# Kernel tuning notes

Hardware: AMD Instinct MI355X
Metric: run time of the kernel (lower is better)

## Reference

```python
import jax, jax.numpy as jnp
from jax import lax
import numpy as np
from functools import partial

B, C, H, W = 4, 3, 256, 256
HW = H * W
KCAP = 32          # max tracked components per (batch, class) slot
MAX_ITER = 5
KSIZE = 5


def _depthwise_sum(x, k):
    c = x.shape[1]
    w = jnp.ones((c, 1, k, k), x.dtype)
    return lax.conv_general_dilated(x, w, (1, 1), [(k // 2, k // 2)] * 2,
                                    feature_group_count=c,
                                    dimension_numbers=('NCHW', 'OIHW', 'NCHW'))


def erode(x):
    return (_depthwise_sum(x, KSIZE) >= KSIZE * KSIZE - 0.5).astype(x.dtype)


def dilate(x):
    return (_depthwise_sum(x, KSIZE) > 0.5).astype(x.dtype)


def _maxpool3_int(L):
    return lax.reduce_window(L, jnp.int32(0), lax.max, (1, 1, 3, 3), (1, 1, 1, 1),
                             [(0, 0), (0, 0), (1, 1), (1, 1)])


def label_cc(binary):
    # connected-component labeling by iterated 3x3 max-pool of pixel indices,
    # exactly as find_components_max_pool (labels = max flat pixel index in comp)
    b = lax.stop_gradient(binary) > 0.5
    idx = jnp.arange(HW, dtype=jnp.int32).reshape(1, 1, H, W)
    L0 = jnp.where(b, idx, 0)

    def cond(st):
        return st[1]

    def body(st):
        L, _ = st
        Ln = jnp.where(b, _maxpool3_int(L), 0)
        return Ln, jnp.any(Ln != L)

    L, _ = lax.while_loop(cond, body, (L0, jnp.array(True)))
    return L


def extract_components(Lf, binf):
    # per (b,c): top-KCAP components sorted by comp.sum() = size*label/maxL (desc)
    flat = Lf.reshape(-1)
    sizes = jnp.zeros((HW,), jnp.float32).at[flat].add(binf.reshape(-1))
    idx = jnp.arange(HW, dtype=jnp.int32)
    is_root = (flat == idx) & (flat > 0)  # label 0 excluded, as in torch code
    key = jnp.where(is_root, lax.stop_gradient(sizes) * idx.astype(jnp.float32), -1.0)
    _, top_lab = lax.top_k(key, KCAP)
    valid = key[top_lab] > 0.0
    maxL = jnp.maximum(flat.max(), 1).astype(jnp.float32)
    v = top_lab.astype(jnp.float32)
    s = jnp.where(valid, sizes[top_lab] * v / maxL, 0.0)  # comp.sum()
    lab = jnp.where(valid, top_lab, -1)
    # component tensor = mask * label/maxL, exactly mask*L/max(L) of the original
    comps = (Lf[None] == lab[:, None, None]).astype(jnp.float32) * (v / maxL)[:, None, None]
    return s, comps, valid


def process_step(P, n, bar, s, comps, valid, t):
    # overlaps vs components stored BEFORE this step; new comps within a step
    # are pixel-disjoint so they can never match each other (overlap == 0).
    OV = jnp.einsum('jhw,khw->jk', comps, P)

    def body(carry, inp):
        P, n, bar = carry
        s_j, comp_j, valid_j, ov_j = inp
        best = jnp.argmax(ov_j)
        matched = ov_j[best] > 0.0
        widx = jnp.clip(jnp.where(matched, best, n), 0, KCAP - 1)
        can = valid_j & (matched | (n < KCAP))
        bar = bar.at[widx, t].set(jnp.where(can, s_j, bar[widx, t]))
        add = valid_j & (~matched) & (n < KCAP)
        nw = jnp.minimum(n, KCAP - 1)
        P = P.at[nw].set(jnp.where(add, comp_j, P[nw]))
        return (P, n + add.astype(n.dtype), bar), None

    (P, n, bar), _ = lax.scan(body, (P, n, bar), (s, comps, valid, OV))
    return P, n, bar


def compute_barcodes(binary):
    half = MAX_ITER // 2
    seq = [(binary, half)]
    m = binary
    for t in range(half):
        m = erode(m)
        seq.append((m, half + t + 1))
    m = binary
    for t in range(half):
        m = dilate(m)
        seq.append((m, half - t - 1))
    BC = B * C
    P = jnp.zeros((BC, KCAP, H, W), jnp.float32)
    n = jnp.zeros((BC,), jnp.int32)
    bar = jnp.zeros((BC, KCAP, MAX_ITER), jnp.float32)
    for mp, t in seq:  # fixed 5-step schedule (structural loop)
        L = label_cc(mp).reshape(BC, H, W)
        s, comps, valid = jax.vmap(extract_components)(L, mp.reshape(BC, H, W))
        P, n, bar = jax.vmap(partial(process_step, t=t))(P, n, bar, s, comps, valid)
    return bar.reshape(B, C, KCAP, MAX_ITER), n.reshape(B, C)


def topo_forward(predictions, gumbel, targets):
    y_soft = jax.nn.softmax(predictions + gumbel, axis=1)
    hard = jax.nn.one_hot(jnp.argmax(y_soft, axis=1), C, axis=1, dtype=jnp.float32)
    binary_pred = hard + y_soft - lax.stop_gradient(y_soft)  # straight-through
    binary_tgt = jnp.moveaxis(jax.nn.one_hot(targets, C, dtype=jnp.float32), -1, 1)
    bp, n_p = compute_barcodes(binary_pred)
    bt, n_t = compute_barcodes(binary_tgt)
    k = jnp.arange(KCAP)
    valid_p = k[None, None] < n_p[:, :, None]
    has_t = k[None, None] < n_t[:, :, None]
    pmax = bp.max(-1)
    pmax = jnp.where(pmax > 0, pmax, 1.0)
    tgt = jnp.where(has_t[..., None], bt, 0.0)
    term = jnp.sum((tgt - bp) ** 2, -1) / pmax ** 2
    losses = jnp.sum(jnp.where(valid_p, term, 0.0), axis=(1, 2))
    return losses.mean()  # reduction='mean'


def setup_inputs() -> dict:
    key = jax.random.key(0)
    k1, k2, k3 = jax.random.split(key, 3)
    # blob-like logits: low-res noise upsampled so component counts stay < KCAP
    lo = jax.random.normal(k1, (B, C, 16, 16), jnp.float32)
    predictions = 8.0 * jax.image.resize(lo, (B, C, H, W), 'linear')
    lo_t = jax.random.normal(k2, (B, C, 16, 16), jnp.float32)
    targets = jnp.argmax(jax.image.resize(lo_t, (B, C, H, W), 'linear'), axis=1).astype(jnp.int32)
    u = jax.random.uniform(k3, (B, C, H, W), jnp.float32, minval=1e-6, maxval=1.0 - 1e-6)
    gumbel = -jnp.log(-jnp.log(u))  # standard Gumbel noise (F.gumbel_softmax)
    return {"predictions": predictions, "gumbel": gumbel, "targets": targets}


def reference(predictions, gumbel, targets):
    return topo_forward(predictions, gumbel, targets)
```

## Files before the change

### kernel.cpp

```cpp
#include <hip/hip_runtime.h>

#define NB 4
#define NC 3
#define BC 12
#define HW 65536
#define KCAP 32
#define MAXI 5
#define RUNCAP 16384
#define NSLOT 120
#define NCH 24

typedef unsigned long long u64;
typedef unsigned int u32;

__device__ __forceinline__ int uf_find(int* P, int x){
  while (true){
    int p = P[x];
    if (p == x) return x;
    int gp = P[p];
    if (gp == p) return p;
    P[x] = gp;
    x = gp;
  }
}
__device__ __forceinline__ void uf_union_max(int* P, int a, int b){
  while (true){
    a = uf_find(P, a); b = uf_find(P, b);
    if (a == b) return;
    if (a > b){ int t = a; a = b; b = t; }
    int old = atomicCAS(&P[a], a, b);
    if (old == a) return;
    a = old;
  }
}

template<typename F>
__device__ __forceinline__ void walk_runs(const u64* wv, F&& emit){
  int open_s = -1;
  #pragma unroll
  for (int wi = 0; wi < 4; wi++){
    u64 v = wv[wi];
    int base = wi << 6;
    int pos = 0;
    while (pos < 64){
      u64 rem = v >> pos;
      if (open_s >= 0){
        u64 nz = ~rem;
        int z = nz ? __builtin_ctzll(nz) : 64;
        if (z >= 64 - pos){ pos = 64; }
        else { emit(open_s, base + pos + z); open_s = -1; pos += z; }
      } else {
        if (rem == 0ull){ pos = 64; }
        else {
          int o = __builtin_ctzll(rem);
          open_s = base + pos + o;
          pos += o;
        }
      }
    }
  }
  if (open_s >= 0) emit(open_s, 256);
}

__global__ void k_bin(const float* __restrict__ pred, const float* __restrict__ gum,
                      const int* __restrict__ tgt, u64* __restrict__ bmAll){
  int g = blockIdx.x * 256 + threadIdx.x;
  int b = g >> 16, p = g & (HW - 1);
  size_t base = (size_t)b * NC * HW + p;
  float v0 = pred[base]        + gum[base];
  float v1 = pred[base + HW]   + gum[base + HW];
  float v2 = pred[base + 2*HW] + gum[base + 2*HW];
  int a = 0; float m = v0;
  if (v1 > m){ m = v1; a = 1; }
  if (v2 > m){ m = v2; a = 2; }
  int tg = tgt[(size_t)b * HW + p];
  u64 p0 = __ballot(a == 0), p1 = __ballot(a == 1), p2 = __ballot(a == 2);
  u64 t0 = __ballot(tg == 0), t1 = __ballot(tg == 1), t2 = __ballot(tg == 2);
  if ((threadIdx.x & 63) == 0){
    int w = p >> 6;
    int sp = b * NC;
    bmAll[(size_t)(sp + 0) * 1024 + w] = p0;
    bmAll[(size_t)(sp + 1) * 1024 + w] = p1;
    bmAll[(size_t)(sp + 2) * 1024 + w] = p2;
    int st = 60 + b * NC;
    bmAll[(size_t)(st + 0) * 1024 + w] = t0;
    bmAll[(size_t)(st + 1) * 1024 + w] = t1;
    bmAll[(size_t)(st + 2) * 1024 + w] = t2;
  }
}

__global__ void k_morph4(const u64* __restrict__ bmAll, u64* __restrict__ bmAllW,
                         int4 srcs, int4 dsts, int4 flgs){
  int t = blockIdx.x * 256 + threadIdx.x;
  int job = t / 12288, rest = t % 12288;
  int s = rest >> 10, word = rest & 1023;
  int row = word >> 2, w = word & 3;
  int srcG = job == 0 ? srcs.x : job == 1 ? srcs.y : job == 2 ? srcs.z : srcs.w;
  int dstG = job == 0 ? dsts.x : job == 1 ? dsts.y : job == 2 ? dsts.z : dsts.w;
  int er   = job == 0 ? flgs.x : job == 1 ? flgs.y : job == 2 ? flgs.z : flgs.w;
  const u64* bs = bmAll + (size_t)(srcG * BC + s) * 1024;
  u64 res = er ? ~0ull : 0ull;
  for (int dy = -2; dy <= 2; dy++){
    int y = row + dy;
    if (y < 0 || y > 255){ if (er) res = 0; continue; }
    const u64* rw = bs + y * 4;
    u64 m = rw[w];
    u64 l = (w > 0) ? rw[w-1] : 0ull;
    u64 r = (w < 3) ? rw[w+1] : 0ull;
    u64 x1l = (m << 1) | (l >> 63);
    u64 x2l = (m << 2) | (l >> 62);
    u64 x1r = (m >> 1) | (r << 63);
    u64 x2r = (m >> 2) | (r << 62);
    u64 h = er ? (m & x1l & x2l & x1r & x2r) : (m | x1l | x2l | x1r | x2r);
    res = er ? (res & h) : (res | h);
  }
  bmAllW[(size_t)(dstG * BC + s) * 1024 + word] = res;
}

__global__ __launch_bounds__(1024) void k_cc_runs(
    const u64* __restrict__ bmAll, u32* __restrict__ selRuns,
    int* __restrict__ selCnt, float* __restrict__ sSel, float* __restrict__ scaleSel){
  __shared__ int par[RUNCAP];
  __shared__ u32 pkz[RUNCAP];
  __shared__ int rs[257];
  __shared__ u64 wcand[16*KCAP];
  __shared__ u64 selKeys[KCAP];
  __shared__ int selRoot[KCAP];
  __shared__ int wsum[4], wsum2[4];
  __shared__ int lmS;
  int u = blockIdx.x, t = threadIdx.x;
  int lane = t & 63, wid = t >> 6;
  bool rowT = t < 256;
  u64 wv[4] = {0,0,0,0};
  int nr = 0;
  if (rowT){
    const u64* bp = bmAll + (size_t)u * 1024 + t * 4;
    #pragma unroll
    for (int i = 0; i < 4; i++) wv[i] = bp[i];
    walk_runs(wv, [&](int a, int b){ (void)a; (void)b; nr++; });
  }
  if (t == 0) lmS = 0;
  {
    int v = nr;
    #pragma unroll
    for (int d = 1; d < 64; d <<= 1){
      int o = __shfl_up(v, d);
      if (lane >= d) v += o;
    }
    if (rowT && lane == 63) wsum[wid] = v;
    __syncthreads();
    if (rowT){
      int pre = 0;
      for (int q = 0; q < wid; q++) pre += wsum[q];
      rs[t] = pre + v - nr;
      if (t == 255) rs[256] = pre + v;
    }
    __syncthreads();
  }
  int NR = rs[256];
  int NRc = NR < RUNCAP ? NR : RUNCAP;
  int myBase = rowT ? rs[t] : 0;
  for (int i = t; i < NRc; i += 1024) par[i] = i;
  if (rowT){
    int o = myBase;
    walk_runs(wv, [&](int a, int b){
      if (o < RUNCAP) pkz[o] = ((u32)t << 16) | ((u32)a << 8) | (u32)(b - 1);
      o++;
    });
  }
  __syncthreads();
  for (int i = t; i < NRc; i += 1024){
    u32 v = pkz[i];
    int r = v >> 16;
    if (r == 0) continue;
    int s2 = (int)((v >> 8) & 255), E2 = (int)(v & 255);
    int a0 = rs[r-1], a1 = rs[r];
    if (a1 > NRc) a1 = NRc;
    if (a0 >= a1) continue;
    int lo = a0, hi = a1;
    while (lo < hi){
      int mid = (lo + hi) >> 1;
      if ((int)(pkz[mid] & 255) >= s2 - 1) hi = mid; else lo = mid + 1;
    }
    for (int j = lo; j < a1; j++){
      int s1 = (int)((pkz[j] >> 8) & 255);
      if (s1 > E2 + 1) break;
      uf_union_max(par, i, j);
    }
  }
  __syncthreads();
  for (int i = t; i < NRc; i += 1024){
    int r = i, p = par[r];
    while (p != r){ r = p; p = par[r]; }
    par[i] = r;
  }
  __syncthreads();
  {
    int lm = 0;
    for (int i0 = 0; i0 < NRc; i0 += 1024){
      int i = i0 + t;
      int root = -1, len = 0;
      if (i < NRc){
        u32 v = pkz[i];
        int s0 = (int)((v >> 8) & 255), E = (int)(v & 255);
        len = E - s0 + 1;
        root = par[i] & 16383;
        lm = max(lm, (int)(v >> 16) * 256 + E);
      }
      int val = len;
      int prev = __shfl_up(root, 1);
      unsigned flg = (lane == 0 || prev != root) ? 1u : 0u;
      #pragma unroll
      for (int d = 1; d < 64; d <<= 1){
        int ov = __shfl_up(val, d);
        unsigned of = __shfl_up(flg, d);
        if (lane >= d){
          if (!flg) val += ov;
          flg |= of;
        }
      }
      int nroot = __shfl_down(root, 1);
      bool last = (lane == 63) || (nroot != root);
      if (i < NRc && last) atomicAdd(&par[root], val << 14);
    }
    #pragma unroll
    for (int off = 32; off > 0; off >>= 1) lm = max(lm, __shfl_xor(lm, off));
    if (lane == 0) atomicMax(&lmS, lm);
  }
  __syncthreads();
  float maxLf = (float)(lmS >= 1 ? lmS : 1);
  for (int i = t; i < NRc; i += 1024){
    int pv = par[i];
    if ((pv & 16383) == i){
      u32 v = pkz[i];
      int lab = (int)(v >> 16) * 256 + (int)(v & 255);
      if (lab > 0){
        float key = (float)((u32)pv >> 14) * (float)lab;
        pkz[i] = __float_as_uint(key);
        par[i] = (lab << 14) | i;
      } else {
        pkz[i] = 0;
      }
    }
  }
  __syncthreads();
  {
    u64 myBest = 0;
    for (int i = t; i < NRc; i += 1024){
      int pv = par[i];
      if ((pv & 16383) != i) continue;
      u32 kh = pkz[i];
      if (!kh) continue;
      u64 cand = ((u64)kh << 32) | ((u64)(0xFFFFu - ((u32)pv >> 14)) << 16) | (u64)i;
      if (cand > myBest) myBest = cand;
    }
    if (lane < KCAP) wcand[wid*KCAP + lane] = 0;
    for (int r = 0; r < KCAP; r++){
      u64 b = myBest;
      #pragma unroll
      for (int off = 32; off > 0; off >>= 1){
        u64 o = __shfl_xor(b, off);
        b = (o > b) ? o : b;
      }
      if (b == 0) break;
      if (lane == 0) wcand[wid*KCAP + r] = b;
      if (myBest == b){
        pkz[(int)(b & 16383)] = 0;
        myBest = 0;
        for (int i = t; i < NRc; i += 1024){
          int pv = par[i];
          if ((pv & 16383) != i) continue;
          u32 kh = pkz[i];
          if (!kh) continue;
          u64 cand = ((u64)kh << 32) | ((u64)(0xFFFFu - ((u32)pv >> 14)) << 16) | (u64)i;
          if (cand > myBest) myBest = cand;
        }
      }
    }
  }
  __syncthreads();
  if (wid == 0){
    u64 c[8];
    #pragma unroll
    for (int q = 0; q < 8; q++) c[q] = wcand[q*64 + lane];
    if (lane < KCAP) selKeys[lane] = 0;
    for (int r = 0; r < KCAP; r++){
      u64 b = 0;
      #pragma unroll
      for (int q = 0; q < 8; q++) b = (c[q] > b) ? c[q] : b;
      #pragma unroll
      for (int off = 32; off > 0; off >>= 1){
        u64 o = __shfl_xor(b, off);
        b = (o > b) ? o : b;
      }
      if (b == 0) break;
      #pragma unroll
      for (int q = 0; q < 8; q++) if (c[q] == b) c[q] = 0;
      if (lane == 0) selKeys[r] = b;
    }
  }
  __syncthreads();
  if (t < KCAP){
    u64 k = selKeys[t];
    if (k){
      int lab = 0xFFFF - (int)((k >> 16) & 0xFFFF);
      selRoot[t] = (int)(k & 0x3FFF);
      sSel[u*KCAP + t]     = __uint_as_float((u32)(k >> 32)) / maxLf;
      scaleSel[u*KCAP + t] = (float)lab / maxLf;
    } else {
      selRoot[t] = -1;
      sSel[u*KCAP + t] = 0.0f;
      scaleSel[u*KCAP + t] = 0.0f;
    }
  }
  __syncthreads();
  for (int i = t; i < NRc; i += 1024) pkz[i] = 255u;
  __syncthreads();
  if (t < KCAP && selRoot[t] >= 0) pkz[selRoot[t]] = (u32)t;
  __syncthreads();
  int c = 0;
  if (rowT){
    int o = myBase;
    walk_runs(wv, [&](int a, int b){
      if (o < RUNCAP && pkz[par[o] & 16383] < KCAP) c++;
      o++;
    });
  }
  {
    int v = c;
    #pragma unroll
    for (int d = 1; d < 64; d <<= 1){
      int o = __shfl_up(v, d);
      if (lane >= d) v += o;
    }
    if (rowT && lane == 63) wsum2[wid] = v;
    __syncthreads();
    if (rowT){
      int pre = 0;
      for (int q = 0; q < wid; q++) pre += wsum2[q];
      int w = pre + v - c;
      size_t base = (size_t)u * RUNCAP;
      int o = myBase;
      walk_runs(wv, [&](int a, int b){
        if (o < RUNCAP){
          u32 j = pkz[par[o] & 16383];
          if (j < KCAP){
            selRuns[base + w] = (j << 24) | ((u32)t << 16) | ((u32)a << 8) | (u32)(b - 1);
            w++;
          }
        }
        o++;
      });
    }
    if (t == 0) selCnt[u] = wsum2[0] + wsum2[1] + wsum2[2] + wsum2[3];
  }
}

__global__ __launch_bounds__(1024) void k_chainall(
    const u32* __restrict__ selRuns, const int* __restrict__ selCnt,
    const float* __restrict__ sSel, const float* __restrict__ scaleSel,
    float* __restrict__ barP, float* __restrict__ barT,
    int* __restrict__ n24, u64* __restrict__ PbT){
  int w = blockIdx.x, t = threadIdx.x;
  int pass = w / 12, s = w % 12;
  __shared__ int cnt[16*KCAP*KCAP];
  __shared__ float spL[KCAP];
  __shared__ int add_dst[KCAP];
  __shared__ int bestA[KCAP];
  __shared__ float bvA[KCAP];
  __shared__ int nS;
  if (t < KCAP) spL[t] = 0.0f;
  if (t == 0) nS = 0;
  float* bar = (pass ? barT : barP) + (size_t)s * KCAP * MAXI;
  u64* Pb = PbT + (size_t)w * KCAP * 1024;
  int g = t >> 5, k = t & 31;
  int wid = t >> 6;
  #pragma unroll 1
  for (int st = 0; st < 5; st++){
    int u = (pass * 5 + st) * BC + s;
    int tval = (st < 3) ? st + 2 : (st == 3 ? 1 : 0);
    for (int i = t; i < 16*KCAP*KCAP; i += 1024) cnt[i] = 0;
    __syncthreads();
    int n0 = nS;
    int NS = selCnt[u];
    const u32* rp = selRuns + (size_t)u * RUNCAP;
    if (n0 > 0){
      for (int i = g; i < NS; i += 32){
        u32 v = rp[i];
        int j = v >> 24;
        int row = (v >> 16) & 255, s0 = (v >> 8) & 255, E = (int)(v & 255);
        int w0 = s0 >> 6, w1 = E >> 6;
        int acc = 0;
        if (k < n0){
          for (int wi = w0; wi <= w1; wi++){
            int lo = max(s0, wi << 6), hi = min(E + 1, (wi << 6) + 64);
            u64 mask = (hi - lo == 64) ? ~0ull : ((((u64)1 << (hi - lo)) - 1) << (lo - (wi << 6)));
            acc += __popcll(Pb[(size_t)(row * 4 + wi) * KCAP + k] & mask);
          }
          if (acc) atomicAdd(&cnt[wid*KCAP*KCAP + j*KCAP + k], acc);
        }
      }
    }
    __syncthreads();
    {
      int tot = 0;
      #pragma unroll
      for (int wq = 0; wq < 16; wq++) tot += cnt[wq*KCAP*KCAP + t];
      cnt[t] = tot;
    }
    __syncthreads();
    if (t < KCAP){
      float sn = scaleSel[(size_t)u*KCAP + t];
      int best = 0; float bv = 0.0f;
      if (sn > 0.0f && n0 > 0){
        bv = sn * spL[0] * (float)cnt[t*KCAP + 0];
        for (int k2 = 1; k2 < n0; k2++){
          float ov = sn * spL[k2] * (float)cnt[t*KCAP + k2];
          if (ov > bv){ bv = ov; best = k2; }
        }
      }
      bestA[t] = best; bvA[t] = bv;
    }
    __syncthreads();
    if (t == 0){
      int n = n0;
      for (int j = 0; j < KCAP; j++){
        add_dst[j] = -1;
        float sv = scaleSel[(size_t)u*KCAP + j];
        if (sv <= 0.0f) continue;
        if (bvA[j] > 0.0f){
          bar[bestA[j]*MAXI + tval] = sSel[(size_t)u*KCAP + j];
        } else if (n < KCAP){
          bar[n*MAXI + tval] = sSel[(size_t)u*KCAP + j];
          spL[n] = sv;
          add_dst[j] = n;
          n++;
        }
      }
      nS = n;
    }
    __syncthreads();
    for (int j = 0; j < KCAP; j++){
      int d = add_dst[j];
      if (d < 0) continue;
      for (int x = t; x < 1024; x += 1024) Pb[(size_t)x * KCAP + d] = 0ull;
    }
    __syncthreads();
    for (int i = t; i < NS; i += 1024){
      u32 v = rp[i];
      int j = v >> 24;
      int d = add_dst[j];
      if (d < 0) continue;
      int row = (v >> 16) & 255, s0 = (v >> 8) & 255, E = (int)(v & 255);
      int w0 = s0 >> 6, w1 = E >> 6;
      for (int wi = w0; wi <= w1; wi++){
        int lo = max(s0, wi << 6), hi = min(E + 1, (wi << 6) + 64);
        u64 mask = (hi - lo == 64) ? ~0ull : ((((u64)1 << (hi - lo)) - 1) << (lo - (wi << 6)));
        atomicOr(&Pb[(size_t)(row * 4 + wi) * KCAP + d], mask);
      }
    }
    __syncthreads();
  }
  if (t == 0) n24[w] = nS;
}

__global__ void k_loss(const float* __restrict__ barP, const float* __restrict__ barT,
                       const int* __restrict__ n24, float* __restrict__ out){
  __shared__ float red[512];
  int t = threadIdx.x;
  float val = 0.0f;
  if (t < BC * KCAP){
    int s = t >> 5, k = t & 31;
    int np = n24[s], nt = n24[12 + s];
    if (k < np){
      const float* bp = barP + (size_t)(s*KCAP + k)*MAXI;
      float pmax = bp[0];
      #pragma unroll
      for (int q = 1; q < MAXI; q++) pmax = fmaxf(pmax, bp[q]);
      if (!(pmax > 0.0f)) pmax = 1.0f;
      float acc = 0.0f;
      #pragma unroll
      for (int q = 0; q < MAXI; q++){
        float tv = (k < nt) ? barT[(size_t)(s*KCAP + k)*MAXI + q] : 0.0f;
        float d = tv - bp[q];
        acc += d * d;
      }
      val = acc / (pmax * pmax);
    }
  }
  red[t] = val;
  __syncthreads();
  for (int off = 256; off > 0; off >>= 1){
    if (t < off) red[t] += red[t + off];
    __syncthreads();
  }
  if (t == 0) out[0] = red[0] * 0.25f;
}

extern "C" void kernel_launch(void* const* d_in, const int* in_sizes, int n_in,
                              void* d_out, int out_size, void* d_ws, size_t ws_size,
                              hipStream_t stream){
  const float* pred = (const float*)d_in[0];
  const float* gum  = (const float*)d_in[1];
  const int*   tgt  = (const int*)d_in[2];
  float* out = (float*)d_out;
  char* ws = (char*)d_ws;
  size_t off = 0;
  auto alloc = [&](size_t bytes)->char*{
    char* p = ws + off;
    off += (bytes + 255) & ~(size_t)255;
    return p;
  };
  u64* bmAll   = (u64*)alloc((size_t)NSLOT*1024*8);
  u32* selRuns = (u32*)alloc((size_t)NSLOT*RUNCAP*4);
  int* selCnt  = (int*)alloc(NSLOT*4);
  float* sSel     = (float*)alloc((size_t)NSLOT*KCAP*4);
  float* scaleSel = (float*)alloc((size_t)NSLOT*KCAP*4);
  u64* PbT     = (u64*)alloc((size_t)NCH*KCAP*1024*8);
  int* n24     = (int*)alloc(NCH*4);
  size_t zbytes = (size_t)(BC*KCAP*MAXI*2)*4;
  char* zreg = alloc(zbytes);
  float* barP = (float*)zreg;
  float* barT = barP + BC*KCAP*MAXI;
  if (off > ws_size) return;

  hipMemsetAsync(zreg, 0, zbytes, stream);
  k_bin<<<(NB*HW)/256,256,0,stream>>>(pred, gum, tgt, bmAll);
  k_morph4<<<192,256,0,stream>>>(bmAll, bmAll, make_int4(0,0,5,5), make_int4(1,3,6,8), make_int4(1,0,1,0));
  k_morph4<<<192,256,0,stream>>>(bmAll, bmAll, make_int4(1,3,6,8), make_int4(2,4,7,9), make_int4(1,0,1,0));
  k_cc_runs<<<NSLOT,1024,0,stream>>>(bmAll, selRuns, selCnt, sSel, scaleSel);
  k_chainall<<<NCH,1024,0,stream>>>(selRuns, selCnt, sSel, scaleSel, barP, barT, n24, PbT);
  k_loss<<<1,512,0,stream>>>(barP, barT, n24, out);
}
```

Measured before the change: 308.6 us.

## Build new component bitmasks in LDS and unroll overlap run loop by four

```diff
diff --git a/kernel.cpp b/kernel.cpp
--- a/kernel.cpp
+++ b/kernel.cpp
@@ -356,25 +356,27 @@
   }
 }
 
-__global__ __launch_bounds__(1024) void k_chainall(
+__global__ __launch_bounds__(1024, 4) void k_chainall(
     const u32* __restrict__ selRuns, const int* __restrict__ selCnt,
     const float* __restrict__ sSel, const float* __restrict__ scaleSel,
     float* __restrict__ barP, float* __restrict__ barT,
     int* __restrict__ n24, u64* __restrict__ PbT){
   int w = blockIdx.x, t = threadIdx.x;
   int pass = w / 12, s = w % 12;
-  __shared__ int cnt[16*KCAP*KCAP];
+  __shared__ u64 shbuf[8192];
   __shared__ float spL[KCAP];
   __shared__ int add_dst[KCAP];
   __shared__ int bestA[KCAP];
   __shared__ float bvA[KCAP];
   __shared__ int nS;
+  int* cnt = (int*)shbuf;
   if (t < KCAP) spL[t] = 0.0f;
   if (t == 0) nS = 0;
   float* bar = (pass ? barT : barP) + (size_t)s * KCAP * MAXI;
   u64* Pb = PbT + (size_t)w * KCAP * 1024;
   int g = t >> 5, k = t & 31;
   int wid = t >> 6;
+  int cw = wid * KCAP * KCAP;
   #pragma unroll 1
   for (int st = 0; st < 5; st++){
     int u = (pass * 5 + st) * BC + s;
@@ -384,28 +386,41 @@
     int n0 = nS;
     int NS = selCnt[u];
     const u32* rp = selRuns + (size_t)u * RUNCAP;
+    #define OVRUN(vv, jj, aacc) { \
+      jj = (int)((vv) >> 24); aacc = 0; \
+      if (jj < KCAP && k < n0){ \
+        int row_ = ((vv) >> 16) & 255, s0_ = ((vv) >> 8) & 255, E_ = (int)((vv) & 255); \
+        int w0_ = s0_ >> 6, w1_ = E_ >> 6; \
+        for (int wi_ = w0_; wi_ <= w1_; wi_++){ \
+          int lo_ = max(s0_, wi_ << 6), hi_ = min(E_ + 1, (wi_ << 6) + 64); \
+          u64 m_ = (hi_ - lo_ == 64) ? ~0ull : ((((u64)1 << (hi_ - lo_)) - 1) << (lo_ - (wi_ << 6))); \
+          aacc += __popcll(Pb[(size_t)(row_ * 4 + wi_) * KCAP + k] & m_); \
+        } \
+      } }
     if (n0 > 0){
-      for (int i = g; i < NS; i += 32){
-        u32 v = rp[i];
-        int j = v >> 24;
-        int row = (v >> 16) & 255, s0 = (v >> 8) & 255, E = (int)(v & 255);
-        int w0 = s0 >> 6, w1 = E >> 6;
-        int acc = 0;
-        if (k < n0){
-          for (int wi = w0; wi <= w1; wi++){
-            int lo = max(s0, wi << 6), hi = min(E + 1, (wi << 6) + 64);
-            u64 mask = (hi - lo == 64) ? ~0ull : ((((u64)1 << (hi - lo)) - 1) << (lo - (wi << 6)));
-            acc += __popcll(Pb[(size_t)(row * 4 + wi) * KCAP + k] & mask);
-          }
-          if (acc) atomicAdd(&cnt[wid*KCAP*KCAP + j*KCAP + k], acc);
-        }
-      }
-    }
+      for (int i = g; i < NS; i += 128){
+        u32 va = rp[i];
+        u32 vb = (i + 32 < NS) ? rp[i + 32] : 0xFFFFFFFFu;
+        u32 vc = (i + 64 < NS) ? rp[i + 64] : 0xFFFFFFFFu;
+        u32 vd = (i + 96 < NS) ? rp[i + 96] : 0xFFFFFFFFu;
+        int j0, j1, j2, j3, a0, a1, a2, a3;
+        OVRUN(va, j0, a0);
+        OVRUN(vb, j1, a1);
+        OVRUN(vc, j2, a2);
+        OVRUN(vd, j3, a3);
+        if (a0) atomicAdd(&cnt[cw + j0*KCAP + k], a0);
+        if (a1) atomicAdd(&cnt[cw + j1*KCAP + k], a1);
+        if (a2) atomicAdd(&cnt[cw + j2*KCAP + k], a2);
+        if (a3) atomicAdd(&cnt[cw + j3*KCAP + k], a3);
+      }
+    }
+    #undef OVRUN
     __syncthreads();
     {
       int tot = 0;
       #pragma unroll
       for (int wq = 0; wq < 16; wq++) tot += cnt[wq*KCAP*KCAP + t];
+      __syncthreads();
       cnt[t] = tot;
     }
     __syncthreads();
@@ -440,24 +455,29 @@
       nS = n;
     }
     __syncthreads();
-    for (int j = 0; j < KCAP; j++){
-      int d = add_dst[j];
-      if (d < 0) continue;
-      for (int x = t; x < 1024; x += 1024) Pb[(size_t)x * KCAP + d] = 0ull;
-    }
-    __syncthreads();
-    for (int i = t; i < NS; i += 1024){
-      u32 v = rp[i];
-      int j = v >> 24;
-      int d = add_dst[j];
-      if (d < 0) continue;
-      int row = (v >> 16) & 255, s0 = (v >> 8) & 255, E = (int)(v & 255);
-      int w0 = s0 >> 6, w1 = E >> 6;
-      for (int wi = w0; wi <= w1; wi++){
-        int lo = max(s0, wi << 6), hi = min(E + 1, (wi << 6) + 64);
-        u64 mask = (hi - lo == 64) ? ~0ull : ((((u64)1 << (hi - lo)) - 1) << (lo - (wi << 6)));
-        atomicOr(&Pb[(size_t)(row * 4 + wi) * KCAP + d], mask);
-      }
+    int nTot = nS;
+    for (int b0 = n0; b0 < nTot; b0 += 8){
+      int bcnt = min(8, nTot - b0);
+      for (int x = t; x < 8192; x += 1024) shbuf[x] = 0ull;
+      __syncthreads();
+      for (int i = t; i < NS; i += 1024){
+        u32 v = rp[i];
+        int j = v >> 24;
+        if (j >= KCAP) continue;
+        int d = add_dst[j];
+        if (d < b0 || d >= b0 + bcnt) continue;
+        int row = (v >> 16) & 255, s0 = (v >> 8) & 255, E = (int)(v & 255);
+        int w0 = s0 >> 6, w1 = E >> 6;
+        for (int wi = w0; wi <= w1; wi++){
+          int lo = max(s0, wi << 6), hi = min(E + 1, (wi << 6) + 64);
+          u64 mask = (hi - lo == 64) ? ~0ull : ((((u64)1 << (hi - lo)) - 1) << (lo - (wi << 6)));
+          atomicOr(&shbuf[(size_t)(row * 4 + wi) * 8 + (d - b0)], mask);
+        }
+      }
+      __syncthreads();
+      for (int dd = 0; dd < bcnt; dd++)
+        Pb[(size_t)t * KCAP + b0 + dd] = shbuf[(size_t)t * 8 + dd];
+      __syncthreads();
     }
     __syncthreads();
   }
```

New measurement: 271.0 us. -12.2%, faster.
